# Kernel optimization log

Measured on AMD Instinct MI355X. Metric: run time of the kernel, lower is better.

Reference implementation:

```python
import jax, jax.numpy as jnp
import numpy as np

DELTA_VAR = 0.5
DELTA_DIST = 1.5
ALPHA = 1.0
BETA = 1.0
C = 4096        # number of superpixels (static for segment_sum)
NE = 16384      # number of RAG edges


def setup_inputs() -> dict:
    key = jax.random.key(0)
    k1, k2, k3, k4 = jax.random.split(key, 4)
    embeddings = jax.random.normal(k1, (1, 16, 1024, 1024), dtype=jnp.float32)
    sp_seg = jax.random.randint(k2, (1, 1, 1024, 1024), 0, C)
    edges = jax.random.randint(k3, (2, NE), 0, C)
    weights = jax.random.uniform(k4, (NE,), dtype=jnp.float32)
    return {"embeddings": embeddings, "weights": weights, "sp_seg": sp_seg, "edges": edges}


def reference(embeddings, weights, sp_seg, edges):
    # embeddings: (1,E,H,W); sp_seg: (1,1,H,W) int labels in [0,C)
    E = embeddings.shape[1]
    emb = embeddings.reshape(E, -1).T          # (P,E) pixel-major
    seg = sp_seg.reshape(-1)                   # (P,)
    counts = jax.ops.segment_sum(jnp.ones(seg.shape, emb.dtype), seg, num_segments=C)  # (C,)
    sums = jax.ops.segment_sum(emb, seg, num_segments=C)                               # (C,E)
    n = jnp.maximum(counts, 1.0)               # guard empty segments (orig would div-by-0)
    means = sums / n[:, None]                  # (C,E) superpixel mean embeddings
    # intra-superpixel: d = 1 - <mean_c, emb_p> at pixels of segment c, hinge at delta_var,
    # normalized per-pixel by segment size, then averaged over C
    d_intra = 1.0 - jnp.sum(means[seg] * emb, axis=-1)            # (P,)
    intra = jnp.sum(jnp.maximum(d_intra - DELTA_VAR, 0.0) / n[seg]) / C
    # inter-superpixel: gather edge endpoint means, weighted hinge at delta_dist
    u, v = edges[0], edges[1]
    d_inter = 1.0 - jnp.sum(means[u] * means[v], axis=-1)         # (Ne,)
    inter = jnp.sum(jnp.maximum(DELTA_DIST - d_inter * weights, 0.0)) / edges.shape[1]
    return ALPHA * inter + BETA * intra
```

## Files before the change

### kernel.cpp

```cpp
#include <hip/hip_runtime.h>

#define C_SEG 4096
#define E_CH 16
#define NE_EDGES 16384
#define P_PIX (1024 * 1024)
#define NCHUNK 64
#define CHUNK_PIX (P_PIX / NCHUNK)
#define SCALE 262144.0f
#define INV_SCALE (1.0f / 262144.0f)


__global__ __launch_bounds__(512, 8) void kA(const float* __restrict__ emb,
                                             const int* __restrict__ seg,
                                             float* __restrict__ sums_part,
                                             float* __restrict__ cnt_part) {
    __shared__ int bins[C_SEG];
    const int vb = blockIdx.x;
    const int t = threadIdx.x;
    const bool is_cnt = (vb >= 1024);
    const int chunk = is_cnt ? (vb - 1024) : (vb & 63);
    const int base = chunk * CHUNK_PIX;

    for (int i = t; i < C_SEG; i += 512) bins[i] = 0;
    __syncthreads();

    if (!is_cnt) {
        const int ch = vb >> 6;
        const float* ec = emb + (size_t)ch * P_PIX;
        int idx = base + t * 4;
        int4 s4 = *(const int4*)(seg + idx);
        float4 v = *(const float4*)(ec + idx);
#pragma unroll
        for (int it = 0; it < 8; ++it) {
            const int4 s4c = s4;
            const float4 vc = v;
            if (it < 7) {
                idx += 512 * 4;
                s4 = *(const int4*)(seg + idx);
                v = *(const float4*)(ec + idx);
            }
            atomicAdd(&bins[s4c.x], __float2int_rn(vc.x * SCALE));
            atomicAdd(&bins[s4c.y], __float2int_rn(vc.y * SCALE));
            atomicAdd(&bins[s4c.z], __float2int_rn(vc.z * SCALE));
            atomicAdd(&bins[s4c.w], __float2int_rn(vc.w * SCALE));
        }
        __syncthreads();
        float* dst = sums_part + ((size_t)ch * NCHUNK + chunk) * C_SEG;
        for (int i = t; i < C_SEG; i += 512)
            dst[i] = (float)bins[i] * INV_SCALE;
    } else {
#pragma unroll
        for (int it = 0; it < 8; ++it) {
            const int idx = base + (it * 512 + t) * 4;
            const int4 s4 = *(const int4*)(seg + idx);
            atomicAdd(&bins[s4.x], 1);
            atomicAdd(&bins[s4.y], 1);
            atomicAdd(&bins[s4.z], 1);
            atomicAdd(&bins[s4.w], 1);
        }
        __syncthreads();
        float* cd = cnt_part + (size_t)chunk * C_SEG;
        for (int i = t; i < C_SEG; i += 512) cd[i] = (float)bins[i];
    }
}

__global__ __launch_bounds__(256) void kB(const float* __restrict__ sums_part,
                                          const float* __restrict__ cnt_part,
                                          float* __restrict__ msum,
                                          float* __restrict__ inv_n) {
    const int vb = blockIdx.x, t = threadIdx.x;
    if (vb < 256) {
        const int c = vb >> 4;
        const int s = (vb & 15) * 256 + t;
        const float* src = sums_part + (size_t)c * NCHUNK * C_SEG + s;
        float acc = 0.0f;
#pragma unroll
        for (int k = 0; k < NCHUNK; ++k) acc += src[(size_t)k * C_SEG];
        msum[s * E_CH + c] = acc;
    } else {
        const int s = (vb - 256) * 256 + t;
        float acc = 0.0f;
#pragma unroll
        for (int k = 0; k < NCHUNK; ++k) acc += cnt_part[(size_t)k * C_SEG + s];
        inv_n[s] = 1.0f / fmaxf(acc, 1.0f);
    }
}

__global__ __launch_bounds__(256, 4) void kC(const float* __restrict__ emb,
                                             const int* __restrict__ seg,
                                             const int* __restrict__ edges,
                                             const float* __restrict__ w,
                                             const float* __restrict__ msum,
                                             const float* __restrict__ inv_n,
                                             float* __restrict__ part) {
    const int b = blockIdx.x, t = threadIdx.x;
    const int q = b * 256 + t;
    const int4 s4 = *(const int4*)(seg + q * 4);
    const float inx = inv_n[s4.x], iny = inv_n[s4.y];
    const float inz = inv_n[s4.z], inw = inv_n[s4.w];
    const float4* emb4 = (const float4*)emb;
    const float4* rA = (const float4*)(msum + s4.x * E_CH);
    const float4* rB = (const float4*)(msum + s4.y * E_CH);
    const float4* rC = (const float4*)(msum + s4.z * E_CH);
    const float4* rD = (const float4*)(msum + s4.w * E_CH);

    float dx = 0.f, dy = 0.f, dz = 0.f, dw = 0.f;
#pragma unroll
    for (int j = 0; j < 4; ++j) {
        const float4 a = rA[j], b4 = rB[j], c4 = rC[j], d4 = rD[j];
        const float* aF = (const float*)&a;
        const float* bF = (const float*)&b4;
        const float* cF = (const float*)&c4;
        const float* dF = (const float*)&d4;
#pragma unroll
        for (int cc = 0; cc < 4; ++cc) {
            const float4 e = emb4[(size_t)(j * 4 + cc) * (P_PIX / 4) + q];
            dx = fmaf(e.x, aF[cc], dx);
            dy = fmaf(e.y, bF[cc], dy);
            dz = fmaf(e.z, cF[cc], dz);
            dw = fmaf(e.w, dF[cc], dw);
        }
    }
    float v = (fmaxf(0.5f - inx * dx, 0.0f) * inx +
               fmaxf(0.5f - iny * dy, 0.0f) * iny +
               fmaxf(0.5f - inz * dz, 0.0f) * inz +
               fmaxf(0.5f - inw * dw, 0.0f) * inw) *
              (1.0f / (float)C_SEG);

    if (t < 16) {
        const int e = b * 16 + t;
        const int u = edges[e];
        const int vv = edges[NE_EDGES + e];
        const float4* mu = (const float4*)(msum + u * E_CH);
        const float4* mv = (const float4*)(msum + vv * E_CH);
        float dot = 0.0f;
#pragma unroll
        for (int j = 0; j < 4; ++j) {
            const float4 a = mu[j];
            const float4 bb = mv[j];
            dot = fmaf(a.x, bb.x, dot);
            dot = fmaf(a.y, bb.y, dot);
            dot = fmaf(a.z, bb.z, dot);
            dot = fmaf(a.w, bb.w, dot);
        }
        const float d = 1.0f - inv_n[u] * inv_n[vv] * dot;
        v += fmaxf(1.5f - d * w[e], 0.0f) * (1.0f / (float)NE_EDGES);
    }

    for (int o = 32; o > 0; o >>= 1) v += __shfl_down(v, o, 64);
    __shared__ float red[4];
    if ((t & 63) == 0) red[t >> 6] = v;
    __syncthreads();
    if (t == 0) part[b] = red[0] + red[1] + red[2] + red[3];
}

__global__ __launch_bounds__(256) void kF(const float* __restrict__ part,
                                          float* __restrict__ out) {
    float v = 0.0f;
    for (int i = threadIdx.x; i < 1024; i += 256) v += part[i];
    for (int o = 32; o > 0; o >>= 1) v += __shfl_down(v, o, 64);
    __shared__ float red[4];
    const int t = threadIdx.x;
    if ((t & 63) == 0) red[t >> 6] = v;
    __syncthreads();
    if (t == 0) out[0] = red[0] + red[1] + red[2] + red[3];
}

extern "C" void kernel_launch(void* const* d_in, const int* in_sizes, int n_in,
                              void* d_out, int out_size, void* d_ws,
                              size_t ws_size, hipStream_t stream) {
    const float* emb = (const float*)d_in[0];
    const float* weights = (const float*)d_in[1];
    const int* seg = (const int*)d_in[2];
    const int* edges = (const int*)d_in[3];
    float* out = (float*)d_out;

    char* ws = (char*)d_ws;
    float* sums_part = (float*)(ws);
    float* cnt_part = (float*)(ws + 0x1000000);
    float* msum = (float*)(ws + 0x1100000);
    float* invn = (float*)(ws + 0x1140000);
    float* part = (float*)(ws + 0x1144000);

    kA<<<1088, 512, 0, stream>>>(emb, seg, sums_part, cnt_part);
    kB<<<272, 256, 0, stream>>>(sums_part, cnt_part, msum, invn);
    kC<<<1024, 256, 0, stream>>>(emb, seg, edges, weights, msum, invn, part);
    kF<<<1, 256, 0, stream>>>(part, out);
}
```

Before: 149.4 us.

## Halve histogram chunks, use 2D grid, fuse final reduction via last-block counter

The histogram kernel now uses 32 chunks of twice the size in a 2D grid, which halves the partial sums that kB must reduce, and drops the manual prefetch pipelining. The separate final reduction kernel is removed. Instead, the last block of kC, found through an atomic counter that kB resets, sums the per-block partials. This saves one kernel launch and some partial-sum traffic, at the cost of fewer blocks in kA (544 vs 1088) and possibly lower latency hiding.

```diff
diff --git a/kernel.cpp b/kernel.cpp
--- a/kernel.cpp
+++ b/kernel.cpp
@@ -4,53 +4,27 @@
 #define E_CH 16
 #define NE_EDGES 16384
 #define P_PIX (1024 * 1024)
-#define NCHUNK 64
+#define NCHUNK 32
 #define CHUNK_PIX (P_PIX / NCHUNK)
 #define SCALE 262144.0f
 #define INV_SCALE (1.0f / 262144.0f)
 
 
-__global__ __launch_bounds__(512, 8) void kA(const float* __restrict__ emb,
-                                             const int* __restrict__ seg,
-                                             float* __restrict__ sums_part,
-                                             float* __restrict__ cnt_part) {
+__global__ __launch_bounds__(512) void kA(const float* __restrict__ emb,
+                                          const int* __restrict__ seg,
+                                          float* __restrict__ sums_part,
+                                          float* __restrict__ cnt_part) {
     __shared__ int bins[C_SEG];
-    const int vb = blockIdx.x;
+    const int chunk = blockIdx.x;
+    const int g = blockIdx.y;
     const int t = threadIdx.x;
-    const bool is_cnt = (vb >= 1024);
-    const int chunk = is_cnt ? (vb - 1024) : (vb & 63);
     const int base = chunk * CHUNK_PIX;
 
     for (int i = t; i < C_SEG; i += 512) bins[i] = 0;
     __syncthreads();
 
-    if (!is_cnt) {
-        const int ch = vb >> 6;
-        const float* ec = emb + (size_t)ch * P_PIX;
-        int idx = base + t * 4;
-        int4 s4 = *(const int4*)(seg + idx);
-        float4 v = *(const float4*)(ec + idx);
-#pragma unroll
-        for (int it = 0; it < 8; ++it) {
-            const int4 s4c = s4;
-            const float4 vc = v;
-            if (it < 7) {
-                idx += 512 * 4;
-                s4 = *(const int4*)(seg + idx);
-                v = *(const float4*)(ec + idx);
-            }
-            atomicAdd(&bins[s4c.x], __float2int_rn(vc.x * SCALE));
-            atomicAdd(&bins[s4c.y], __float2int_rn(vc.y * SCALE));
-            atomicAdd(&bins[s4c.z], __float2int_rn(vc.z * SCALE));
-            atomicAdd(&bins[s4c.w], __float2int_rn(vc.w * SCALE));
-        }
-        __syncthreads();
-        float* dst = sums_part + ((size_t)ch * NCHUNK + chunk) * C_SEG;
-        for (int i = t; i < C_SEG; i += 512)
-            dst[i] = (float)bins[i] * INV_SCALE;
-    } else {
-#pragma unroll
-        for (int it = 0; it < 8; ++it) {
+    if (g == 16) {
+        for (int it = 0; it < 16; ++it) {
             const int idx = base + (it * 512 + t) * 4;
             const int4 s4 = *(const int4*)(seg + idx);
             atomicAdd(&bins[s4.x], 1);
@@ -61,14 +35,31 @@
         __syncthreads();
         float* cd = cnt_part + (size_t)chunk * C_SEG;
         for (int i = t; i < C_SEG; i += 512) cd[i] = (float)bins[i];
+    } else {
+        const float* ec = emb + (size_t)g * P_PIX;
+        for (int it = 0; it < 16; ++it) {
+            const int idx = base + (it * 512 + t) * 4;
+            const int4 s4 = *(const int4*)(seg + idx);
+            const float4 v = *(const float4*)(ec + idx);
+            atomicAdd(&bins[s4.x], __float2int_rn(v.x * SCALE));
+            atomicAdd(&bins[s4.y], __float2int_rn(v.y * SCALE));
+            atomicAdd(&bins[s4.z], __float2int_rn(v.z * SCALE));
+            atomicAdd(&bins[s4.w], __float2int_rn(v.w * SCALE));
+        }
+        __syncthreads();
+        float* dst = sums_part + ((size_t)g * NCHUNK + chunk) * C_SEG;
+        for (int i = t; i < C_SEG; i += 512)
+            dst[i] = (float)bins[i] * INV_SCALE;
     }
 }
 
 __global__ __launch_bounds__(256) void kB(const float* __restrict__ sums_part,
                                           const float* __restrict__ cnt_part,
                                           float* __restrict__ msum,
-                                          float* __restrict__ inv_n) {
+                                          float* __restrict__ inv_n,
+                                          int* __restrict__ counter) {
     const int vb = blockIdx.x, t = threadIdx.x;
+    if (vb == 0 && t == 0) *counter = 0;
     if (vb < 256) {
         const int c = vb >> 4;
         const int s = (vb & 15) * 256 + t;
@@ -92,7 +83,9 @@
                                              const float* __restrict__ w,
                                              const float* __restrict__ msum,
                                              const float* __restrict__ inv_n,
-                                             float* __restrict__ part) {
+                                             float* __restrict__ part,
+                                             int* __restrict__ counter,
+                                             float* __restrict__ out) {
     const int b = blockIdx.x, t = threadIdx.x;
     const int q = b * 256 + t;
     const int4 s4 = *(const int4*)(seg + q * 4);
@@ -149,21 +142,26 @@
 
     for (int o = 32; o > 0; o >>= 1) v += __shfl_down(v, o, 64);
     __shared__ float red[4];
+    __shared__ int lastflag;
     if ((t & 63) == 0) red[t >> 6] = v;
     __syncthreads();
-    if (t == 0) part[b] = red[0] + red[1] + red[2] + red[3];
-}
-
-__global__ __launch_bounds__(256) void kF(const float* __restrict__ part,
-                                          float* __restrict__ out) {
-    float v = 0.0f;
-    for (int i = threadIdx.x; i < 1024; i += 256) v += part[i];
-    for (int o = 32; o > 0; o >>= 1) v += __shfl_down(v, o, 64);
-    __shared__ float red[4];
-    const int t = threadIdx.x;
-    if ((t & 63) == 0) red[t >> 6] = v;
+    if (t == 0) {
+        part[b] = red[0] + red[1] + red[2] + red[3];
+        __threadfence();
+        lastflag = (atomicAdd(counter, 1) == 1023);
+    }
     __syncthreads();
-    if (t == 0) out[0] = red[0] + red[1] + red[2] + red[3];
+    if (lastflag) {
+        __threadfence();
+        const volatile float* pv = part;
+        float f = 0.0f;
+        for (int i = t; i < 1024; i += 256) f += pv[i];
+        for (int o = 32; o > 0; o >>= 1) f += __shfl_down(f, o, 64);
+        __syncthreads();
+        if ((t & 63) == 0) red[t >> 6] = f;
+        __syncthreads();
+        if (t == 0) out[0] = red[0] + red[1] + red[2] + red[3];
+    }
 }
 
 extern "C" void kernel_launch(void* const* d_in, const int* in_sizes, int n_in,
@@ -177,13 +175,15 @@
 
     char* ws = (char*)d_ws;
     float* sums_part = (float*)(ws);
-    float* cnt_part = (float*)(ws + 0x1000000);
-    float* msum = (float*)(ws + 0x1100000);
-    float* invn = (float*)(ws + 0x1140000);
-    float* part = (float*)(ws + 0x1144000);
+    float* cnt_part = (float*)(ws + 0x800000);
+    float* msum = (float*)(ws + 0x880000);
+    float* invn = (float*)(ws + 0x8C0000);
+    float* part = (float*)(ws + 0x8C4000);
+    int* counter = (int*)(ws + 0x8C5000);
 
-    kA<<<1088, 512, 0, stream>>>(emb, seg, sums_part, cnt_part);
-    kB<<<272, 256, 0, stream>>>(sums_part, cnt_part, msum, invn);
-    kC<<<1024, 256, 0, stream>>>(emb, seg, edges, weights, msum, invn, part);
-    kF<<<1, 256, 0, stream>>>(part, out);
+    dim3 gA(NCHUNK, 17);
+    kA<<<gA, 512, 0, stream>>>(emb, seg, sums_part, cnt_part);
+    kB<<<272, 256, 0, stream>>>(sums_part, cnt_part, msum, invn, counter);
+    kC<<<1024, 256, 0, stream>>>(emb, seg, edges, weights, msum, invn, part,
+                                 counter, out);
 }
```

New measurement: 164.8 us. 10.3% more time.
